# Optimization experiments

Hardware: AMD Instinct MI355X
Metric: run time of the kernel (lower is better)

Reference implementation:

```python
import jax, jax.numpy as jnp
import numpy as np


def setup_inputs() -> dict:
    key = jax.random.key(0)
    k1, k2, k3, k4, k5 = jax.random.split(key, 5)
    B, S, D_IN, D_OUT = 4, 2048, 4096, 4096
    inp = jax.random.normal(k1, (B, S, D_IN), dtype=jnp.float32)
    w_q = jax.random.randint(k2, (D_OUT, D_IN), 0, 255, dtype=jnp.int32)
    scale = jax.random.uniform(k3, (D_OUT, 1), dtype=jnp.float32) * 0.02 + 1e-3
    zero_point = jax.random.randint(k4, (D_OUT, 1), 0, 255, dtype=jnp.int32)
    bias = jax.random.normal(k5, (D_OUT,), dtype=jnp.float32)
    return {"input": inp, "w_q": w_q, "scale": scale, "zero_point": zero_point, "bias": bias}


def reference(input, w_q, scale, zero_point, bias):
    # decompress_module: dequantize int weight with per-output-channel affine params
    # W[o, i] = (w_q[o, i] - zp[o]) * scale[o]   -> full fp32 weight materialized
    W = (w_q - zero_point).astype(jnp.float32) * scale  # [D_OUT, D_IN]
    # F.linear: y = x @ W^T + b
    return jnp.einsum("bsi,oi->bso", input, W) + bias
```

## Files before the change

kernel.cpp:

```cpp
#include <hip/hip_runtime.h>
#include <hip/hip_bf16.h>
#include <stdint.h>

typedef float  f32x4  __attribute__((ext_vector_type(4)));
typedef float  f32x16 __attribute__((ext_vector_type(16)));
typedef unsigned int   u32x4 __attribute__((ext_vector_type(4)));
typedef unsigned short u16x4 __attribute__((ext_vector_type(4)));
typedef int    i32x4  __attribute__((ext_vector_type(4)));

__device__ inline unsigned short f2bf(float f) {
  unsigned int u = __builtin_bit_cast(unsigned int, f);
  u += 0x7fffu + ((u >> 16) & 1u);
  return (unsigned short)(u >> 16);
}

__device__ inline void mfma32x32x16bf16(f32x16& acc, u32x4 a, u32x4 b) {
  asm volatile("v_mfma_f32_32x32x16_bf16 %0, %1, %2, %0"
               : "+v"(acc)
               : "v"(a), "v"(b));
}

__device__ inline void mfma16x16x32bf16(f32x4& acc, u32x4 a, u32x4 b) {
  asm volatile("v_mfma_f32_16x16x32_bf16 %0, %1, %2, %0"
               : "+v"(acc)
               : "v"(a), "v"(b));
}

__device__ inline void gload16(const unsigned short* src, char* ldsdst) {
  __builtin_amdgcn_global_load_lds(
      (const __attribute__((address_space(1))) void*)src,
      (__attribute__((address_space(3))) void*)ldsdst, 16, 0, 0);
}


__global__ __launch_bounds__(256) void prep_x(const float* __restrict__ x,
                                              unsigned short* __restrict__ xb,
                                              int K, int KT) {
  const int rb = blockIdx.x / KT;
  const int kt = blockIdx.x % KT;
  __shared__ unsigned short t[256 * 64];
  const int tid = threadIdx.x;
  const int klane = tid & 15;
  const int rbase = tid >> 4;
  const float* src = x + (size_t)(rb * 256) * K + kt * 64;
  const int gw = klane >> 1, hw = klane & 1;
  for (int it = 0; it < 16; ++it) {
    int row = it * 16 + rbase;
    f32x4 v = *(const f32x4*)(src + (size_t)row * K + klane * 4);
    u16x4 h;
    h[0] = f2bf(v[0]); h[1] = f2bf(v[1]); h[2] = f2bf(v[2]); h[3] = f2bf(v[3]);
    *(u16x4*)&t[row * 64 + ((gw ^ (row & 7)) << 3) + hw * 4] = h;
  }
  __syncthreads();
  unsigned short* dst = xb + ((size_t)rb * KT + kt) * 16384;
  for (int j = 0; j < 8; ++j) {
    int c = j * 256 + tid;
    int l = c & 63, f = (c >> 6) & 7, s = c >> 9;
    int row = f * 32 + (l & 31);
    int g   = (s * 2 + (l >> 5)) ^ (row & 7);
    u32x4 v = *(const u32x4*)&t[row * 64 + (g << 3)];
    *(u32x4*)(dst + (size_t)c * 8) = v;
  }
}

__global__ __launch_bounds__(256) void prep_w(const int* __restrict__ wq,
                                              const int* __restrict__ zp,
                                              unsigned short* __restrict__ wb,
                                              int K, int KT) {
  const int cb = blockIdx.x / KT;
  const int kt = blockIdx.x % KT;
  __shared__ unsigned short t[256 * 64];
  const int tid = threadIdx.x;
  const int klane = tid & 15;
  const int rbase = tid >> 4;
  const int* src = wq + (size_t)(cb * 256) * K + kt * 64;
  const int gw = klane >> 1, hw = klane & 1;
  for (int it = 0; it < 16; ++it) {
    int row = it * 16 + rbase;
    i32x4 v = *(const i32x4*)(src + (size_t)row * K + klane * 4);
    int z = zp[cb * 256 + row];
    u16x4 h;
    h[0] = f2bf((float)(v[0] - z)); h[1] = f2bf((float)(v[1] - z));
    h[2] = f2bf((float)(v[2] - z)); h[3] = f2bf((float)(v[3] - z));
    *(u16x4*)&t[row * 64 + ((gw ^ (row & 7)) << 3) + hw * 4] = h;
  }
  __syncthreads();
  unsigned short* dst = wb + ((size_t)cb * KT + kt) * 16384;
  for (int j = 0; j < 8; ++j) {
    int c = j * 256 + tid;
    int l = c & 63, f = (c >> 6) & 7, s = c >> 9;
    int row = f * 32 + (l & 31);
    int g   = (s * 2 + (l >> 5)) ^ (row & 7);
    u32x4 v = *(const u32x4*)&t[row * 64 + (g << 3)];
    *(u32x4*)(dst + (size_t)c * 8) = v;
  }
}

__global__ __launch_bounds__(512, 2) void gemm_ring(
    const unsigned short* __restrict__ xb, const unsigned short* __restrict__ wb,
    const float* __restrict__ scale, const float* __restrict__ bias,
    float* __restrict__ out, int N, int KT) {

  __shared__ unsigned short lds[32768];

  const int NB = N >> 8;
  const int nwg = gridDim.x;
  const int wg  = (blockIdx.x & 7) * (nwg >> 3) + (blockIdx.x >> 3);
  const int rb = wg / NB;
  const int cb = wg % NB;

  const int tid  = threadIdx.x;
  const int lane = tid & 63;
  const int wave = tid >> 6;
  const int wr = wave >> 2;
  const int wc = wave & 3;
  const int wr4 = wr * 4, wc2 = wc * 2;
  const int lane16 = lane * 16;

  const unsigned short* xtb = xb + (size_t)rb * (KT >> 1) * 16384;
  const unsigned short* wtb = wb + (size_t)cb * (KT >> 1) * 16384;

  f32x16 acc[4][2] = {};
  u32x4 bA[2][2], bB[2][2];

  auto STAGE = [&](int u) {
    const int slot = (u & 3) << 14;
    const unsigned short* as = xtb + (size_t)u * 8192;
    char* da = (char*)lds + slot + wave * 2048;
    gload16(as + wave * 1024 + lane * 8, da);
    gload16(as + wave * 1024 + 512 + lane * 8, da + 1024);
  };

  auto LDA = [&](int slotb, int s, int m) -> u32x4 {
    return *(const u32x4*)((const char*)lds + slotb + s * 8192 +
                           (wr4 + m) * 1024 + lane16);
  };

#define BODY(U, CUR, NXT, VM, DOB, DOS)                                        \
  {                                                                            \
    const int u_ = (U);                                                        \
    const int sb = (u_ & 3) << 14;                                             \
    __builtin_amdgcn_s_barrier();      \
    if (DOB) {                                                                 \
      const unsigned short* bsrc = wtb + (size_t)(u_ + 1) * 8192 + lane * 8;   \
      _Pragma("unroll")                                                        \
      for (int s = 0; s < 2; ++s)                                              \
        _Pragma("unroll")                                                      \
        for (int n = 0; n < 2; ++n)                                            \
          NXT[s][n] = *(const u32x4*)(bsrc + s * 4096 + (wc2 + n) * 512);      \
    }                                                                          \
    if (DOS) STAGE(u_ + 3);                                                    \
    asm volatile("s_waitcnt vmcnt(" #VM ")" ::: "memory");                     \
    __builtin_amdgcn_s_setprio(1);                                             \
    _Pragma("unroll")                                                          \
    for (int s = 0; s < 2; ++s)                                                \
      _Pragma("unroll")                                                        \
      for (int m = 0; m < 4; ++m) {                                            \
        u32x4 a = LDA(sb, s, m);                                               \
        mfma32x32x16bf16(acc[m][0], a, CUR[s][0]);                             \
        mfma32x32x16bf16(acc[m][1], a, CUR[s][1]);                             \
      }                                                                        \
    __builtin_amdgcn_s_setprio(0);                                             \
  }

  {
    const unsigned short* bsrc = wtb + lane * 8;
#pragma unroll
    for (int s = 0; s < 2; ++s)
#pragma unroll
      for (int n = 0; n < 2; ++n)
        bA[s][n] = *(const u32x4*)(bsrc + s * 4096 + (wc2 + n) * 512);
  }
  STAGE(0); STAGE(1); STAGE(2);

  int u = 0;
  for (; u + 4 < KT; u += 2) {
    BODY(u,     bA, bB, 8, true, true);
    BODY(u + 1, bB, bA, 8, true, true);
  }
  BODY(u, bA, bB, 8, true,  true);  ++u;
  BODY(u, bB, bA, 6, true,  false); ++u;
  BODY(u, bA, bB, 4, true,  false); ++u;
  BODY(u, bB, bA, 0, false, false);
#undef BODY

  const int m0 = rb * 256 + wr * 128;
  const int n0 = cb * 256 + wc * 64;
  const int l31 = lane & 31, lhi = lane >> 5;
#pragma unroll
  for (int n = 0; n < 2; ++n) {
    const int col = n0 + n * 32 + l31;
    const float sc = scale[col];
    const float bi = bias[col];
#pragma unroll
    for (int m = 0; m < 4; ++m) {
      f32x16 v = acc[m][n];
      const int rowb = m0 + m * 32 + 4 * lhi;
#pragma unroll
      for (int q = 0; q < 4; ++q)
#pragma unroll
        for (int r = 0; r < 4; ++r)
          out[(size_t)(rowb + q * 8 + r) * N + col] = v[q * 4 + r] * sc + bi;
    }
  }
}

__global__ __launch_bounds__(256) void gemm_fallback(
    const float* __restrict__ x, const int* __restrict__ wq, const int* __restrict__ zp,
    const float* __restrict__ scale, const float* __restrict__ bias,
    float* __restrict__ out, int M, int N, int K) {

  __shared__ unsigned short Alds[128 * 32];
  __shared__ unsigned short Blds[128 * 32];

  const int tid = threadIdx.x;
  const int ntile = N / 128;
  const int m0 = (blockIdx.x / ntile) * 128, n0 = (blockIdx.x % ntile) * 128;
  const int lane = tid & 63;
  const int wave = tid >> 6;
  const int wr = wave >> 1, wc = wave & 1;
  const int lr = lane & 15, lhi = lane >> 4;
  f32x4 acc[4][4] = {};
  const int ar = tid >> 3, ac4 = tid & 7;

  for (int k0 = 0; k0 < K; k0 += 32) {
#pragma unroll
    for (int p = 0; p < 4; ++p) {
      int r = p * 32 + ar;
      i32x4 w = *(const i32x4*)(wq + (size_t)(n0 + r) * K + k0 + ac4 * 4);
      int z = zp[n0 + r];
      u16x4 h;
      h[0] = f2bf((float)(w[0] - z)); h[1] = f2bf((float)(w[1] - z));
      h[2] = f2bf((float)(w[2] - z)); h[3] = f2bf((float)(w[3] - z));
      *(u16x4*)&Blds[r * 32 + ac4 * 4] = h;
    }
#pragma unroll
    for (int p = 0; p < 4; ++p) {
      int r = p * 32 + ar;
      f32x4 v = *(const f32x4*)(x + (size_t)(m0 + r) * K + k0 + ac4 * 4);
      u16x4 h;
      h[0] = f2bf(v[0]); h[1] = f2bf(v[1]); h[2] = f2bf(v[2]); h[3] = f2bf(v[3]);
      *(u16x4*)&Alds[r * 32 + ac4 * 4] = h;
    }
    __syncthreads();
    u32x4 af[4], bf[4];
#pragma unroll
    for (int i = 0; i < 4; ++i) {
      af[i] = *(const u32x4*)&Alds[(wr * 64 + i * 16 + lr) * 32 + lhi * 8];
      bf[i] = *(const u32x4*)&Blds[(wc * 64 + i * 16 + lr) * 32 + lhi * 8];
    }
#pragma unroll
    for (int i = 0; i < 4; ++i)
#pragma unroll
      for (int j = 0; j < 4; ++j)
        mfma16x16x32bf16(acc[i][j], af[i], bf[j]);
    __syncthreads();
  }
  const int crow0 = m0 + wr * 64;
  const int ccol0 = n0 + wc * 64 + lr;
#pragma unroll
  for (int j = 0; j < 4; ++j) {
    int col = ccol0 + j * 16;
    float sc = scale[col], bi = bias[col];
#pragma unroll
    for (int i = 0; i < 4; ++i) {
      int row = crow0 + i * 16 + lhi * 4;
      f32x4 v = acc[i][j];
#pragma unroll
      for (int r = 0; r < 4; ++r)
        out[(size_t)(row + r) * N + col] = v[r] * sc + bi;
    }
  }
}

extern "C" void kernel_launch(void* const* d_in, const int* in_sizes, int n_in,
                              void* d_out, int out_size, void* d_ws, size_t ws_size,
                              hipStream_t stream) {
  const float* x     = (const float*)d_in[0];
  const int*   wq    = (const int*)d_in[1];
  const float* scale = (const float*)d_in[2];
  const int*   zp    = (const int*)d_in[3];
  const float* bias  = (const float*)d_in[4];
  float* out = (float*)d_out;

  const int DOUT = in_sizes[4];
  const int DIN  = in_sizes[1] / DOUT;
  const int M    = in_sizes[0] / DIN;

  const size_t needX = (size_t)M * DIN * 2;
  const size_t needW = (size_t)DOUT * DIN * 2;

  const int nwg  = (M / 256) * (DOUT / 256);
  const int KT64 = DIN / 64;
  const int KT32 = DIN / 32;
  const bool shapes_ok = (M % 256 == 0) && (DOUT % 256 == 0) && (DIN % 64 == 0) &&
                         (nwg % 8 == 0) && (KT32 >= 8) && (KT32 % 2 == 0);

  if (shapes_ok && ws_size >= needX + needW) {
    unsigned short* xb = (unsigned short*)d_ws;
    unsigned short* wb = (unsigned short*)((char*)d_ws + needX);
    prep_x<<<(M / 256) * KT64, 256, 0, stream>>>(x, xb, DIN, KT64);
    prep_w<<<(DOUT / 256) * KT64, 256, 0, stream>>>(wq, zp, wb, DIN, KT64);
    gemm_ring<<<nwg, 512, 0, stream>>>(xb, wb, scale, bias, out, DOUT, KT32);
  } else {
    dim3 grid((M / 128) * (DOUT / 128));
    gemm_fallback<<<grid, 256, 0, stream>>>(x, wq, zp, scale, bias, out, M, DOUT, DIN);
  }
}
```

Before: 326.1 us.

## Load A fragments directly from global into registers, drop LDS ring

Removes the LDS ring buffer that staged activation tiles with global_load_lds and barriers. Each wave now loads both A and B fragments straight from global memory into registers, double-buffered across k-steps. This drops the LDS traffic and block barriers. In exchange, A tiles that were shared across the 4 column-waves are now fetched 4 times from global/L2, register pressure rises, and the prefetch depth falls from 3 stages to 1.

Result: slower. 385.6 us (+18.3%).

```diff
diff --git a/kernel.cpp b/kernel.cpp
--- a/kernel.cpp
+++ b/kernel.cpp
@@ -24,12 +24,6 @@
   asm volatile("v_mfma_f32_16x16x32_bf16 %0, %1, %2, %0"
                : "+v"(acc)
                : "v"(a), "v"(b));
-}
-
-__device__ inline void gload16(const unsigned short* src, char* ldsdst) {
-  __builtin_amdgcn_global_load_lds(
-      (const __attribute__((address_space(1))) void*)src,
-      (__attribute__((address_space(3))) void*)ldsdst, 16, 0, 0);
 }
 
 
@@ -101,8 +95,6 @@
     const float* __restrict__ scale, const float* __restrict__ bias,
     float* __restrict__ out, int N, int KT) {
 
-  __shared__ unsigned short lds[32768];
-
   const int NB = N >> 8;
   const int nwg = gridDim.x;
   const int wg  = (blockIdx.x & 7) * (nwg >> 3) + (blockIdx.x >> 3);
@@ -115,74 +107,54 @@
   const int wr = wave >> 2;
   const int wc = wave & 3;
   const int wr4 = wr * 4, wc2 = wc * 2;
-  const int lane16 = lane * 16;
+  const int lane8 = lane * 8;
 
   const unsigned short* xtb = xb + (size_t)rb * (KT >> 1) * 16384;
   const unsigned short* wtb = wb + (size_t)cb * (KT >> 1) * 16384;
 
   f32x16 acc[4][2] = {};
-  u32x4 bA[2][2], bB[2][2];
-
-  auto STAGE = [&](int u) {
-    const int slot = (u & 3) << 14;
-    const unsigned short* as = xtb + (size_t)u * 8192;
-    char* da = (char*)lds + slot + wave * 2048;
-    gload16(as + wave * 1024 + lane * 8, da);
-    gload16(as + wave * 1024 + 512 + lane * 8, da + 1024);
+
+  struct FragSet { u32x4 a[2][4]; u32x4 b[2][2]; };
+
+  auto LOADSET = [&](FragSet& F, int u) {
+    const unsigned short* xa = xtb + (size_t)u * 8192;
+    const unsigned short* wa = wtb + (size_t)u * 8192;
+#pragma unroll
+    for (int s = 0; s < 2; ++s) {
+#pragma unroll
+      for (int n = 0; n < 2; ++n)
+        F.b[s][n] = *(const u32x4*)(wa + s * 4096 + (wc2 + n) * 512 + lane8);
+#pragma unroll
+      for (int m = 0; m < 4; ++m)
+        F.a[s][m] = *(const u32x4*)(xa + s * 4096 + (wr4 + m) * 512 + lane8);
+    }
   };
 
-  auto LDA = [&](int slotb, int s, int m) -> u32x4 {
-    return *(const u32x4*)((const char*)lds + slotb + s * 8192 +
-                           (wr4 + m) * 1024 + lane16);
+  auto MM = [&](FragSet& F) {
+    __builtin_amdgcn_s_setprio(1);
+#pragma unroll
+    for (int s = 0; s < 2; ++s)
+#pragma unroll
+      for (int m = 0; m < 4; ++m) {
+        mfma32x32x16bf16(acc[m][0], F.a[s][m], F.b[s][0]);
+        mfma32x32x16bf16(acc[m][1], F.a[s][m], F.b[s][1]);
+      }
+    __builtin_amdgcn_s_setprio(0);
   };
 
-#define BODY(U, CUR, NXT, VM, DOB, DOS)                                        \
-  {                                                                            \
-    const int u_ = (U);                                                        \
-    const int sb = (u_ & 3) << 14;                                             \
-    __builtin_amdgcn_s_barrier();      \
-    if (DOB) {                                                                 \
-      const unsigned short* bsrc = wtb + (size_t)(u_ + 1) * 8192 + lane * 8;   \
-      _Pragma("unroll")                                                        \
-      for (int s = 0; s < 2; ++s)                                              \
-        _Pragma("unroll")                                                      \
-        for (int n = 0; n < 2; ++n)                                            \
-          NXT[s][n] = *(const u32x4*)(bsrc + s * 4096 + (wc2 + n) * 512);      \
-    }                                                                          \
-    if (DOS) STAGE(u_ + 3);                                                    \
-    asm volatile("s_waitcnt vmcnt(" #VM ")" ::: "memory");                     \
-    __builtin_amdgcn_s_setprio(1);                                             \
-    _Pragma("unroll")                                                          \
-    for (int s = 0; s < 2; ++s)                                                \
-      _Pragma("unroll")                                                        \
-      for (int m = 0; m < 4; ++m) {                                            \
-        u32x4 a = LDA(sb, s, m);                                               \
-        mfma32x32x16bf16(acc[m][0], a, CUR[s][0]);                             \
-        mfma32x32x16bf16(acc[m][1], a, CUR[s][1]);                             \
-      }                                                                        \
-    __builtin_amdgcn_s_setprio(0);                                             \
-  }
-
-  {
-    const unsigned short* bsrc = wtb + lane * 8;
-#pragma unroll
-    for (int s = 0; s < 2; ++s)
-#pragma unroll
-      for (int n = 0; n < 2; ++n)
-        bA[s][n] = *(const u32x4*)(bsrc + s * 4096 + (wc2 + n) * 512);
-  }
-  STAGE(0); STAGE(1); STAGE(2);
+  FragSet fsA, fsB;
+  LOADSET(fsA, 0);
 
   int u = 0;
-  for (; u + 4 < KT; u += 2) {
-    BODY(u,     bA, bB, 8, true, true);
-    BODY(u + 1, bB, bA, 8, true, true);
-  }
-  BODY(u, bA, bB, 8, true,  true);  ++u;
-  BODY(u, bB, bA, 6, true,  false); ++u;
-  BODY(u, bA, bB, 4, true,  false); ++u;
-  BODY(u, bB, bA, 0, false, false);
-#undef BODY
+  for (; u + 2 < KT; u += 2) {
+    LOADSET(fsB, u + 1);
+    MM(fsA);
+    LOADSET(fsA, u + 2);
+    MM(fsB);
+  }
+  LOADSET(fsB, u + 1);
+  MM(fsA);
+  MM(fsB);
 
   const int m0 = rb * 256 + wr * 128;
   const int n0 = cb * 256 + wc * 64;
```
